# Kernel tuning notes

Hardware: AMD Instinct MI355X
Metric: run time of the kernel (lower is better)

The kernel has to match this reference:

```python
import jax, jax.numpy as jnp
import numpy as np

SEQ, IN_DIM, HID_DIM, OUT_DIM, WIDTH, DEPTH = 8192, 1024, 1024, 1024, 2048, 3


def setup_inputs() -> dict:
    key = jax.random.key(0)
    ks = jax.random.split(key, 8)
    s = lambda fi, fo: 1.0 / np.sqrt(fi)  # torch Linear default init scale
    return {
        "x": jax.random.normal(ks[0], (SEQ, IN_DIM), dtype=jnp.float32),
        "W0": jax.random.uniform(ks[1], (IN_DIM + HID_DIM, WIDTH), jnp.float32, -s(IN_DIM + HID_DIM, WIDTH), s(IN_DIM + HID_DIM, WIDTH)),
        "b0": jax.random.uniform(ks[2], (WIDTH,), jnp.float32, -s(IN_DIM + HID_DIM, WIDTH), s(IN_DIM + HID_DIM, WIDTH)),
        "Wmid": jax.random.uniform(ks[3], (DEPTH, WIDTH, WIDTH), jnp.float32, -s(WIDTH, WIDTH), s(WIDTH, WIDTH)),
        "bmid": jax.random.uniform(ks[4], (DEPTH, WIDTH), jnp.float32, -s(WIDTH, WIDTH), s(WIDTH, WIDTH)),
        "Wf": jax.random.uniform(ks[5], (WIDTH, HID_DIM + OUT_DIM), jnp.float32, -s(WIDTH, HID_DIM + OUT_DIM), s(WIDTH, HID_DIM + OUT_DIM)),
        "bf": jax.random.uniform(ks[6], (HID_DIM + OUT_DIM,), jnp.float32, -s(WIDTH, HID_DIM + OUT_DIM), s(WIDTH, HID_DIM + OUT_DIM)),
    }


def _mlp(f, W0, b0, Wmid, bmid, Wf, bf):
    # f: [in_dim + hid_dim]
    h = f @ W0 + b0
    for i in range(DEPTH):  # fixed small depth
        h = jax.nn.relu(h) @ Wmid[i] + bmid[i]
    return jax.nn.relu(h) @ Wf + bf  # [hid_dim + out_dim]


def reference(x, W0, b0, Wmid, bmid, Wf, bf):
    def step(hidden, x_t):
        feat = jnp.concatenate([x_t, hidden], axis=-1)
        o = _mlp(feat, W0, b0, Wmid, bmid, Wf, bf)
        return o[:HID_DIM], o[HID_DIM:]

    hidden0 = jnp.zeros((HID_DIM,), dtype=x.dtype)
    hidden, outputs = jax.lax.scan(step, hidden0, x)
    # match torch: hidden returned with leading singleton batch dim
    return hidden[None, :], outputs
```

## Files before the change

kernel.cpp:

```cpp
#include <hip/hip_runtime.h>
#include <hip/hip_bf16.h>
#include <stdint.h>

#define SEQ     8192
#define DIM     2048
#define HID     1024
#define NWG     256
#define CPW     8

typedef unsigned long long u64;
typedef __attribute__((ext_vector_type(4))) unsigned int u32x4;


__device__ __forceinline__ uint16_t f2bf(float f) {
  union { float f; uint32_t u; } v; v.f = f;
  uint32_t r = v.u + 0x7FFFu + ((v.u >> 16) & 1u);
  return (uint16_t)(r >> 16);
}
__device__ __forceinline__ float bf2f(uint16_t u) {
  union { uint32_t u; float f; } v; v.u = ((uint32_t)u) << 16; return v.f;
}
__device__ __forceinline__ void cstore64(u64* p, u64 v) {
  __hip_atomic_store(p, v, __ATOMIC_RELAXED, __HIP_MEMORY_SCOPE_AGENT);
}
__device__ __forceinline__ u64 pack2(float v0, float v1, uint32_t tag) {
  const uint32_t w0 = (uint32_t)f2bf(v0) | (tag << 16);
  const uint32_t w1 = (uint32_t)f2bf(v1) | (tag << 16);
  return ((u64)w1 << 32) | (u64)w0;
}
__device__ __forceinline__ u32x4 cload128(const void* p) {
  u32x4 r;
  asm volatile("global_load_dwordx4 %0, %1, off sc0 sc1"
               : "=v"(r) : "v"(p) : "memory");
  return r;
}
__device__ __forceinline__ void vm_drain() {
  asm volatile("s_waitcnt vmcnt(0)" ::: "memory");
  __builtin_amdgcn_sched_barrier(0);
}

__device__ __forceinline__ void poll_stage(const uint32_t* __restrict__ buf,
                                           int chunk, uint32_t thr,
                                           float* __restrict__ d) {
  const uint32_t* p = buf + (size_t)chunk * 16;
  u32x4 a, b;
  for (;;) {
    a = cload128(p);
    b = cload128(p + 4);
    vm_drain();
    bool ok = true;
    #pragma unroll
    for (int i = 0; i < 4; ++i) {
      ok &= (a[i] >= thr);
      ok &= (b[i] >= thr);
    }
    if (__all(ok)) break;
    __builtin_amdgcn_s_sleep(1);
  }
  #pragma unroll
  for (int i = 0; i < 4; ++i) {
    d[i]     = fmaxf(__uint_as_float(a[i] << 16), 0.f);
    d[4 + i] = fmaxf(__uint_as_float(b[i] << 16), 0.f);
  }
}

__device__ __forceinline__ void lds_spin(uint32_t* f, uint32_t want) {
  while (__hip_atomic_load(f, __ATOMIC_RELAXED,
                           __HIP_MEMORY_SCOPE_WORKGROUP) < want) {}
  asm volatile("" ::: "memory");
  __builtin_amdgcn_sched_barrier(0);
}

__global__ void k_hb(const float* __restrict__ W0, const float* __restrict__ b0,
                     const float* __restrict__ bfv, float* __restrict__ hb) {
  const int j = blockIdx.x * 256 + threadIdx.x;
  float acc = b0[j];
  for (int m = 0; m < HID; ++m)
    acc = fmaf(bfv[m], W0[(size_t)(HID + m) * DIM + j], acc);
  hb[j] = acc;
}

__global__ void k_G(const float* __restrict__ W0, const float* __restrict__ Wf,
                    float* __restrict__ Gt) {
  const int j = blockIdx.x * 16 + threadIdx.x;
  const int k = blockIdx.y * 16 + threadIdx.y;
  float acc = 0.f;
  for (int m = 0; m < HID; ++m)
    acc = fmaf(Wf[(size_t)k * DIM + m], W0[(size_t)(HID + m) * DIM + j], acc);
  Gt[(size_t)j * DIM + k] = acc;
}

__global__ void k_XC(const float* __restrict__ x, const float* __restrict__ W0,
                     const float* __restrict__ b0, const float* __restrict__ hb,
                     float* __restrict__ out, uint16_t* __restrict__ xct) {
  const int j = blockIdx.x * 16 + threadIdx.x;
  const int t = blockIdx.y * 16 + threadIdx.y;
  float acc = 0.f;
  for (int m = 0; m < HID; ++m)
    acc = fmaf(x[(size_t)t * HID + m], W0[(size_t)m * DIM + j], acc);
  acc += (t > 0) ? hb[j] : b0[j];
  const uint16_t v = f2bf(acc);
  if (t <= SEQ - 3) ((uint16_t*)(out + HID + (size_t)(t + 2) * HID))[j] = v;
  else              xct[(size_t)(t - (SEQ - 2)) * DIM + j] = v;
}

__global__ void __launch_bounds__(256, 1)
rnn_persist(const float* __restrict__ Wmid, const float* __restrict__ bmid,
            const float* __restrict__ Wf, const float* __restrict__ bfv,
            float* __restrict__ out, uint32_t* __restrict__ a0b,
            uint32_t* __restrict__ a1b, uint32_t* __restrict__ a2b,
            uint32_t* __restrict__ a3b, const float* __restrict__ Gt,
            const uint16_t* __restrict__ xct)
{
  __shared__ uint16_t wlds[3 * CPW * DIM];
  __shared__ uint16_t wflds[4 * DIM];
  __shared__ float    sAct[2][DIM];
  __shared__ u64      sG[2][4];
  __shared__ uint32_t sflag[2][4];

  const int tid  = threadIdx.x;
  const int wg   = blockIdx.x;
  const int wave = tid >> 6;
  const int lane = tid & 63;

  const int cidx0 = wave * 2;
  const int col0  = wg * CPW + cidx0;
  const int col1  = col0 + 1;
  const int ocol  = wg * 4 + wave;

  for (int i = tid; i < 3 * CPW * DIM; i += 256) {
    const int l = i >> 14;
    const int r = i & 16383;
    const int k = r >> 3;
    const int c = r & 7;
    wlds[(l * CPW + c) * DIM + k] =
        f2bf(Wmid[(size_t)l * DIM * DIM + (size_t)k * DIM + (wg * CPW + c)]);
  }
  for (int i = tid; i < 4 * DIM; i += 256) {
    const int w = i >> 11;
    const int k = i & 2047;
    wflds[w * DIM + k] = f2bf(Wf[(size_t)k * DIM + HID + wg * 4 + w]);
  }
  float4 gf0[8], gf1[8];
  #pragma unroll
  for (int qi = 0; qi < 4; ++qi) {
    const int q = (wave + qi) & 3;
    #pragma unroll
    for (int jj = 0; jj < 2; ++jj) {
      const int k = (2 * q + jj) * 256 + lane * 4;
      gf0[qi * 2 + jj] = *(const float4*)(Gt + (size_t)col0 * DIM + k);
      gf1[qi * 2 + jj] = *(const float4*)(Gt + (size_t)col1 * DIM + k);
    }
  }
  if (tid < 8) {
    sG[tid >> 2][tid & 3] = 0;
    sflag[tid >> 2][tid & 3] = 0;
  }
  __syncthreads();

  float bm0[3], bm1[3];
  #pragma unroll
  for (int l = 0; l < 3; ++l) {
    bm0[l] = bmid[l * DIM + col0];
    bm1[l] = bmid[l * DIM + col1];
  }
  const float bo = bfv[HID + ocol];

  uint32_t ph = 0;

  for (int t = 0; t < SEQ; ++t) {
    {
      const int par = (int)(ph & 1u);
      float* __restrict__ sa = sAct[par];
      const uint32_t want = ph + 1u;
      const uint16_t* xcrow = (t <= SEQ - 3)
          ? (const uint16_t*)(out + HID + (size_t)(t + 2) * HID)
          : (xct + (size_t)(t - (SEQ - 2)) * DIM);
      const uint32_t xcw = *(const uint32_t*)(xcrow + col0);

      poll_stage(a3b, wave * 64 + lane, (4u * (uint32_t)t) << 16,
                 sa + wave * 512 + lane * 8);
      asm volatile("s_waitcnt lgkmcnt(0)" ::: "memory");
      __builtin_amdgcn_sched_barrier(0);
      if (lane == 0)
        __hip_atomic_store(&sflag[par][wave], want, __ATOMIC_RELAXED,
                           __HIP_MEMORY_SCOPE_WORKGROUP);

      float acc0 = 0.f, acc1 = 0.f, accO = 0.f;
      #pragma unroll
      for (int qi = 0; qi < 4; ++qi) {
        const int q = (wave + qi) & 3;
        if (qi > 0) lds_spin(&sflag[par][q], want);
        #pragma unroll
        for (int jj = 0; jj < 2; ++jj) {
          const int kb = (2 * q + jj) * 256 + lane * 4;
          const float4 a = *(const float4*)&sa[kb];
          const float4 g0 = gf0[qi * 2 + jj], g1 = gf1[qi * 2 + jj];
          const ushort4 wo = *(const ushort4*)(wflds + wave * DIM + kb);
          acc0 = fmaf(a.x, g0.x, acc0); acc1 = fmaf(a.x, g1.x, acc1);
          acc0 = fmaf(a.y, g0.y, acc0); acc1 = fmaf(a.y, g1.y, acc1);
          acc0 = fmaf(a.z, g0.z, acc0); acc1 = fmaf(a.z, g1.z, acc1);
          acc0 = fmaf(a.w, g0.w, acc0); acc1 = fmaf(a.w, g1.w, acc1);
          accO = fmaf(a.x, bf2f(wo.x), accO);
          accO = fmaf(a.y, bf2f(wo.y), accO);
          accO = fmaf(a.z, bf2f(wo.z), accO);
          accO = fmaf(a.w, bf2f(wo.w), accO);
        }
      }
      #pragma unroll
      for (int off = 32; off > 0; off >>= 1) {
        acc0 += __shfl_xor(acc0, off, 64);
        acc1 += __shfl_xor(acc1, off, 64);
        accO += __shfl_xor(accO, off, 64);
      }
      const uint32_t tag = 4u * (uint32_t)t + 1u;
      if (lane == 0) {
        const float v0 = acc0 + bf2f((uint16_t)(xcw & 0xFFFFu));
        const float v1 = acc1 + bf2f((uint16_t)(xcw >> 16));
        __hip_atomic_store(&sG[par][wave], pack2(v0, v1, tag),
                           __ATOMIC_RELAXED, __HIP_MEMORY_SCOPE_WORKGROUP);
        if (t > 0)
          out[HID + (size_t)(t - 1) * HID + ocol] = accO + bo;
      }
      if (wave == 0 && lane < 4) {
        const uint32_t thr = tag << 16;
        u64 pv;
        for (;;) {
          pv = __hip_atomic_load(&sG[par][lane], __ATOMIC_RELAXED,
                                 __HIP_MEMORY_SCOPE_WORKGROUP);
          if ((uint32_t)pv >= thr && (uint32_t)(pv >> 32) >= thr) break;
        }
        cstore64((u64*)a0b + wg * 8 + lane, pv);
      }
      ++ph;
    }
    #pragma unroll
    for (int l = 1; l < 4; ++l) {
      const int par = (int)(ph & 1u);
      float* __restrict__ sa = sAct[par];
      const uint32_t want = ph + 1u;
      const uint32_t* src = (l == 1) ? a0b : ((l == 2) ? a1b : a2b);
      uint32_t* dst = (l == 1) ? a1b : ((l == 2) ? a2b : a3b);
      poll_stage(src, wave * 64 + lane,
                 (4u * (uint32_t)t + (uint32_t)l) << 16,
                 sa + wave * 512 + lane * 8);
      asm volatile("s_waitcnt lgkmcnt(0)" ::: "memory");
      __builtin_amdgcn_sched_barrier(0);
      if (lane == 0)
        __hip_atomic_store(&sflag[par][wave], want, __ATOMIC_RELAXED,
                           __HIP_MEMORY_SCOPE_WORKGROUP);

      float acc0 = 0.f, acc1 = 0.f;
      const uint16_t* w0p = wlds + (((l - 1) * CPW + cidx0) * DIM);
      const uint16_t* w1p = w0p + DIM;
      #pragma unroll
      for (int qi = 0; qi < 4; ++qi) {
        const int q = (wave + qi) & 3;
        if (qi > 0) lds_spin(&sflag[par][q], want);
        #pragma unroll
        for (int jj = 0; jj < 2; ++jj) {
          const int kb = (2 * q + jj) * 256 + lane * 4;
          const float4  a  = *(const float4*)&sa[kb];
          const ushort4 wa = *(const ushort4*)(w0p + kb);
          const ushort4 wb = *(const ushort4*)(w1p + kb);
          acc0 = fmaf(a.x, bf2f(wa.x), acc0); acc1 = fmaf(a.x, bf2f(wb.x), acc1);
          acc0 = fmaf(a.y, bf2f(wa.y), acc0); acc1 = fmaf(a.y, bf2f(wb.y), acc1);
          acc0 = fmaf(a.z, bf2f(wa.z), acc0); acc1 = fmaf(a.z, bf2f(wb.z), acc1);
          acc0 = fmaf(a.w, bf2f(wa.w), acc0); acc1 = fmaf(a.w, bf2f(wb.w), acc1);
        }
      }
      #pragma unroll
      for (int off = 32; off > 0; off >>= 1) {
        acc0 += __shfl_xor(acc0, off, 64);
        acc1 += __shfl_xor(acc1, off, 64);
      }
      const uint32_t tag = 4u * (uint32_t)t + (uint32_t)l + 1u;
      if (lane == 0) {
        __hip_atomic_store(&sG[par][wave],
                           pack2(acc0 + bm0[l - 1], acc1 + bm1[l - 1], tag),
                           __ATOMIC_RELAXED, __HIP_MEMORY_SCOPE_WORKGROUP);
      }
      if (wave == 0 && lane < 4) {
        const uint32_t thr = tag << 16;
        u64 pv;
        for (;;) {
          pv = __hip_atomic_load(&sG[par][lane], __ATOMIC_RELAXED,
                                 __HIP_MEMORY_SCOPE_WORKGROUP);
          if ((uint32_t)pv >= thr && (uint32_t)(pv >> 32) >= thr) break;
        }
        cstore64((u64*)dst + wg * 8 + lane, pv);
      }
      ++ph;
    }
  }

  {
    float* __restrict__ sa = sAct[ph & 1u];
    poll_stage(a3b, wave * 64 + lane, (4u * (uint32_t)SEQ) << 16,
               sa + wave * 512 + lane * 8);
    __syncthreads();
    float accO = 0.f, accH = 0.f;
    #pragma unroll
    for (int j = 0; j < 8; ++j) {
      const int kb = j * 256 + lane * 4;
      const float4  a  = *(const float4*)&sa[kb];
      const ushort4 wo = *(const ushort4*)(wflds + wave * DIM + kb);
      accO = fmaf(a.x, bf2f(wo.x), accO);
      accO = fmaf(a.y, bf2f(wo.y), accO);
      accO = fmaf(a.z, bf2f(wo.z), accO);
      accO = fmaf(a.w, bf2f(wo.w), accO);
      accH = fmaf(a.x, Wf[(size_t)(kb + 0) * DIM + ocol], accH);
      accH = fmaf(a.y, Wf[(size_t)(kb + 1) * DIM + ocol], accH);
      accH = fmaf(a.z, Wf[(size_t)(kb + 2) * DIM + ocol], accH);
      accH = fmaf(a.w, Wf[(size_t)(kb + 3) * DIM + ocol], accH);
    }
    #pragma unroll
    for (int off = 32; off > 0; off >>= 1) {
      accO += __shfl_xor(accO, off, 64);
      accH += __shfl_xor(accH, off, 64);
    }
    if (lane == 0) {
      out[HID + (size_t)(SEQ - 1) * HID + ocol] = accO + bo;
      out[ocol] = accH + bfv[ocol];
    }
  }
}

extern "C" void kernel_launch(void* const* d_in, const int* in_sizes, int n_in,
                              void* d_out, int out_size, void* d_ws, size_t ws_size,
                              hipStream_t stream) {
  (void)in_sizes; (void)n_in; (void)out_size; (void)ws_size;
  const float* x    = (const float*)d_in[0];
  const float* W0   = (const float*)d_in[1];
  const float* b0   = (const float*)d_in[2];
  const float* Wmid = (const float*)d_in[3];
  const float* bmid = (const float*)d_in[4];
  const float* Wf   = (const float*)d_in[5];
  const float* bfv  = (const float*)d_in[6];
  float* out = (float*)d_out;

  uint8_t* ws = (uint8_t*)d_ws;
  uint32_t* a0b = (uint32_t*)(ws + 0);
  uint32_t* a1b = (uint32_t*)(ws + 16384);
  uint32_t* a2b = (uint32_t*)(ws + 32768);
  uint32_t* a3b = (uint32_t*)(ws + 49152);
  uint16_t* xct = (uint16_t*)(ws + 65536);
  float*    hb  = (float*)(ws + 73728);
  float*    Gt  = (float*)(ws + 81920);

  hipMemsetAsync(d_ws, 0, 65536, stream);

  k_hb<<<dim3(8), dim3(256), 0, stream>>>(W0, b0, bfv, hb);
  k_G<<<dim3(128, 128), dim3(16, 16), 0, stream>>>(W0, Wf, Gt);
  k_XC<<<dim3(128, 512), dim3(16, 16), 0, stream>>>(x, W0, b0, hb, out, xct);

  rnn_persist<<<dim3(NWG), dim3(256), 0, stream>>>(
      Wmid, bmid, Wf, bfv, out, a0b, a1b, a2b, a3b, Gt, xct);
}
```

Baseline: 108.7 ms.

## Publish per-wave activations directly to padded global lines, drop LDS gather

Each wave now writes its two packed bf16+tag outputs straight to its own 64-byte-strided global slot, so the per-workgroup LDS staging and the wave-0 spin-and-forward step are gone. Consumers poll four 8-byte loads spread across padded lines instead of two contiguous 16-byte loads. The aim is to shorten the critical path of each layer handoff in the sequential recurrence by removing an intra-workgroup wait. In exchange the activation buffers are four times larger, the memset grows accordingly, and each poll touches more cache lines.

```diff
diff --git a/kernel.cpp b/kernel.cpp
--- a/kernel.cpp
+++ b/kernel.cpp
@@ -9,7 +9,7 @@
 #define CPW     8
 
 typedef unsigned long long u64;
-typedef __attribute__((ext_vector_type(4))) unsigned int u32x4;
+typedef __attribute__((ext_vector_type(2))) unsigned int u32x2;
 
 
 __device__ __forceinline__ uint16_t f2bf(float f) {
@@ -28,9 +28,9 @@
   const uint32_t w1 = (uint32_t)f2bf(v1) | (tag << 16);
   return ((u64)w1 << 32) | (u64)w0;
 }
-__device__ __forceinline__ u32x4 cload128(const void* p) {
-  u32x4 r;
-  asm volatile("global_load_dwordx4 %0, %1, off sc0 sc1"
+__device__ __forceinline__ u32x2 cload64c(const void* p) {
+  u32x2 r;
+  asm volatile("global_load_dwordx2 %0, %1, off sc0 sc1"
                : "=v"(r) : "v"(p) : "memory");
   return r;
 }
@@ -40,28 +40,29 @@
 }
 
 __device__ __forceinline__ void poll_stage(const uint32_t* __restrict__ buf,
-                                           int chunk, uint32_t thr,
+                                           int wave, int lane, uint32_t thr,
                                            float* __restrict__ d) {
-  const uint32_t* p = buf + (size_t)chunk * 16;
-  u32x4 a, b;
+  const uint32_t* p = buf + (size_t)(wave * 256 + lane * 4) * 16;
+  u32x2 a, b, c, e;
   for (;;) {
-    a = cload128(p);
-    b = cload128(p + 4);
+    a = cload64c(p);
+    b = cload64c(p + 16);
+    c = cload64c(p + 32);
+    e = cload64c(p + 48);
     vm_drain();
-    bool ok = true;
-    #pragma unroll
-    for (int i = 0; i < 4; ++i) {
-      ok &= (a[i] >= thr);
-      ok &= (b[i] >= thr);
-    }
+    bool ok = (a[0] >= thr) & (a[1] >= thr) & (b[0] >= thr) & (b[1] >= thr) &
+              (c[0] >= thr) & (c[1] >= thr) & (e[0] >= thr) & (e[1] >= thr);
     if (__all(ok)) break;
     __builtin_amdgcn_s_sleep(1);
   }
-  #pragma unroll
-  for (int i = 0; i < 4; ++i) {
-    d[i]     = fmaxf(__uint_as_float(a[i] << 16), 0.f);
-    d[4 + i] = fmaxf(__uint_as_float(b[i] << 16), 0.f);
-  }
+  d[0] = fmaxf(__uint_as_float(a[0] << 16), 0.f);
+  d[1] = fmaxf(__uint_as_float(a[1] << 16), 0.f);
+  d[2] = fmaxf(__uint_as_float(b[0] << 16), 0.f);
+  d[3] = fmaxf(__uint_as_float(b[1] << 16), 0.f);
+  d[4] = fmaxf(__uint_as_float(c[0] << 16), 0.f);
+  d[5] = fmaxf(__uint_as_float(c[1] << 16), 0.f);
+  d[6] = fmaxf(__uint_as_float(e[0] << 16), 0.f);
+  d[7] = fmaxf(__uint_as_float(e[1] << 16), 0.f);
 }
 
 __device__ __forceinline__ void lds_spin(uint32_t* f, uint32_t want) {
@@ -115,7 +116,6 @@
   __shared__ uint16_t wlds[3 * CPW * DIM];
   __shared__ uint16_t wflds[4 * DIM];
   __shared__ float    sAct[2][DIM];
-  __shared__ u64      sG[2][4];
   __shared__ uint32_t sflag[2][4];
 
   const int tid  = threadIdx.x;
@@ -127,6 +127,7 @@
   const int col0  = wg * CPW + cidx0;
   const int col1  = col0 + 1;
   const int ocol  = wg * 4 + wave;
+  const size_t myline = (size_t)(wg * 4 + wave) * 8;
 
   for (int i = tid; i < 3 * CPW * DIM; i += 256) {
     const int l = i >> 14;
@@ -152,10 +153,7 @@
       gf1[qi * 2 + jj] = *(const float4*)(Gt + (size_t)col1 * DIM + k);
     }
   }
-  if (tid < 8) {
-    sG[tid >> 2][tid & 3] = 0;
-    sflag[tid >> 2][tid & 3] = 0;
-  }
+  if (tid < 8) sflag[tid >> 2][tid & 3] = 0;
   __syncthreads();
 
   float bm0[3], bm1[3];
@@ -178,7 +176,7 @@
           : (xct + (size_t)(t - (SEQ - 2)) * DIM);
       const uint32_t xcw = *(const uint32_t*)(xcrow + col0);
 
-      poll_stage(a3b, wave * 64 + lane, (4u * (uint32_t)t) << 16,
+      poll_stage(a3b, wave, lane, (4u * (uint32_t)t) << 16,
                  sa + wave * 512 + lane * 8);
       asm volatile("s_waitcnt lgkmcnt(0)" ::: "memory");
       __builtin_amdgcn_sched_barrier(0);
@@ -217,20 +215,9 @@
       if (lane == 0) {
         const float v0 = acc0 + bf2f((uint16_t)(xcw & 0xFFFFu));
         const float v1 = acc1 + bf2f((uint16_t)(xcw >> 16));
-        __hip_atomic_store(&sG[par][wave], pack2(v0, v1, tag),
-                           __ATOMIC_RELAXED, __HIP_MEMORY_SCOPE_WORKGROUP);
+        cstore64((u64*)a0b + myline, pack2(v0, v1, tag));
         if (t > 0)
           out[HID + (size_t)(t - 1) * HID + ocol] = accO + bo;
-      }
-      if (wave == 0 && lane < 4) {
-        const uint32_t thr = tag << 16;
-        u64 pv;
-        for (;;) {
-          pv = __hip_atomic_load(&sG[par][lane], __ATOMIC_RELAXED,
-                                 __HIP_MEMORY_SCOPE_WORKGROUP);
-          if ((uint32_t)pv >= thr && (uint32_t)(pv >> 32) >= thr) break;
-        }
-        cstore64((u64*)a0b + wg * 8 + lane, pv);
       }
       ++ph;
     }
@@ -241,8 +228,7 @@
       const uint32_t want = ph + 1u;
       const uint32_t* src = (l == 1) ? a0b : ((l == 2) ? a1b : a2b);
       uint32_t* dst = (l == 1) ? a1b : ((l == 2) ? a2b : a3b);
-      poll_stage(src, wave * 64 + lane,
-                 (4u * (uint32_t)t + (uint32_t)l) << 16,
+      poll_stage(src, wave, lane, (4u * (uint32_t)t + (uint32_t)l) << 16,
                  sa + wave * 512 + lane * 8);
       asm volatile("s_waitcnt lgkmcnt(0)" ::: "memory");
       __builtin_amdgcn_sched_barrier(0);
@@ -275,28 +261,16 @@
         acc1 += __shfl_xor(acc1, off, 64);
       }
       const uint32_t tag = 4u * (uint32_t)t + (uint32_t)l + 1u;
-      if (lane == 0) {
-        __hip_atomic_store(&sG[par][wave],
-                           pack2(acc0 + bm0[l - 1], acc1 + bm1[l - 1], tag),
-                           __ATOMIC_RELAXED, __HIP_MEMORY_SCOPE_WORKGROUP);
-      }
-      if (wave == 0 && lane < 4) {
-        const uint32_t thr = tag << 16;
-        u64 pv;
-        for (;;) {
-          pv = __hip_atomic_load(&sG[par][lane], __ATOMIC_RELAXED,
-                                 __HIP_MEMORY_SCOPE_WORKGROUP);
-          if ((uint32_t)pv >= thr && (uint32_t)(pv >> 32) >= thr) break;
-        }
-        cstore64((u64*)dst + wg * 8 + lane, pv);
-      }
+      if (lane == 0)
+        cstore64((u64*)dst + myline,
+                 pack2(acc0 + bm0[l - 1], acc1 + bm1[l - 1], tag));
       ++ph;
     }
   }
 
   {
     float* __restrict__ sa = sAct[ph & 1u];
-    poll_stage(a3b, wave * 64 + lane, (4u * (uint32_t)SEQ) << 16,
+    poll_stage(a3b, wave, lane, (4u * (uint32_t)SEQ) << 16,
                sa + wave * 512 + lane * 8);
     __syncthreads();
     float accO = 0.f, accH = 0.f;
@@ -341,14 +315,14 @@
 
   uint8_t* ws = (uint8_t*)d_ws;
   uint32_t* a0b = (uint32_t*)(ws + 0);
-  uint32_t* a1b = (uint32_t*)(ws + 16384);
-  uint32_t* a2b = (uint32_t*)(ws + 32768);
-  uint32_t* a3b = (uint32_t*)(ws + 49152);
-  uint16_t* xct = (uint16_t*)(ws + 65536);
-  float*    hb  = (float*)(ws + 73728);
-  float*    Gt  = (float*)(ws + 81920);
-
-  hipMemsetAsync(d_ws, 0, 65536, stream);
+  uint32_t* a1b = (uint32_t*)(ws + 65536);
+  uint32_t* a2b = (uint32_t*)(ws + 131072);
+  uint32_t* a3b = (uint32_t*)(ws + 196608);
+  uint16_t* xct = (uint16_t*)(ws + 262144);
+  float*    hb  = (float*)(ws + 270336);
+  float*    Gt  = (float*)(ws + 278528);
+
+  hipMemsetAsync(d_ws, 0, 262144, stream);
 
   k_hb<<<dim3(8), dim3(256), 0, stream>>>(W0, b0, bfv, hb);
   k_G<<<dim3(128, 128), dim3(16, 16), 0, stream>>>(W0, Wf, Gt);
```

Measured after the change: 185.9 ms. 71.1% more time.
